# Optimization experiments

Hardware: AMD Instinct MI355X
Metric: run time of the kernel (lower is better)

## Reference

```python
import jax, jax.numpy as jnp
import numpy as np

GELU = lambda x: jax.nn.gelu(x, approximate=False)  # torch nn.GELU default (erf)
BN_EPS = 1e-5

def _conv(x, w, pad):
    return jax.lax.conv_general_dilated(x, w, (1, 1), pad,
                                        dimension_numbers=('NCHW', 'OIHW', 'NCHW'))

def setup_inputs() -> dict:
    B, D, L = 4096, 768, 3
    IC, R = D // 2, 16  # FDA intermediate channels, reduction ratio
    ks = iter(jax.random.split(jax.random.key(0), 64))
    def nrm(shape, s=0.02):
        return jax.random.normal(next(ks), shape, jnp.float32) * s
    z = lambda *s: jnp.zeros(s, jnp.float32)
    o = lambda *s: jnp.ones(s, jnp.float32)
    inp = {
        'text_feature': jax.random.normal(next(ks), (B, D), jnp.float32),
        'image_feature': jax.random.normal(next(ks), (B, D), jnp.float32),
        'tl_w': nrm((D, D)), 'tl_b': z(D),
        'il_w': nrm((D, D)), 'il_b': z(D),
        'sda_wq': nrm((512, D)), 'sda_bq': z(512),
        'sda_wk': nrm((512, D)), 'sda_bk': z(512),
        'sda_wv': nrm((512, D)), 'sda_bv': z(512),
        'sda_wo': nrm((D, 512)), 'sda_bo': z(D),
        'fda_w1': nrm((IC, D, 3, 3)), 'fda_b1': z(IC),
        'fda_bn1_g': o(IC), 'fda_bn1_b': z(IC),
        'fda_ca_w1': nrm((IC // R, IC, 1, 1)), 'fda_ca_w2': nrm((IC, IC // R, 1, 1)),
        'fda_sa_w': nrm((1, IC, 7, 7)), 'fda_sa_b': z(1),
        'fda_dec_w': nrm((1, IC, 1, 1)), 'fda_dec_b': z(1),
        'fda_sigma': jnp.full((1, IC, 1, 1), 1e-5, jnp.float32),
        'fda_wf': nrm((D, IC, 1, 1)), 'fda_bf': z(D),
        'fda_bn2_g': o(D), 'fda_bn2_b': z(D),
        'dmi_wq': nrm((D, D)), 'dmi_bq': z(D),
        'dmi_wk': nrm((D, D)), 'dmi_bk': z(D),
        'dmi_wv': nrm((D, D)), 'dmi_bv': z(D),
        'tg_w1': nrm((D, D)), 'tg_b1': z(D),
        'tg_w2': nrm((D, D)), 'tg_b2': z(D),
        'ig_w1': nrm((D, D)), 'ig_b1': z(D),
        'ig_w2': nrm((D, D)), 'ig_b2': z(D),
        'text_scale': o(1, D), 'image_scale': o(1, D),
        'cls_w': nrm((L, D)), 'cls_b': z(L),
    }
    return inp

def reference(text_feature, image_feature, tl_w, tl_b, il_w, il_b,
              sda_wq, sda_bq, sda_wk, sda_bk, sda_wv, sda_bv, sda_wo, sda_bo,
              fda_w1, fda_b1, fda_bn1_g, fda_bn1_b, fda_ca_w1, fda_ca_w2,
              fda_sa_w, fda_sa_b, fda_dec_w, fda_dec_b, fda_sigma,
              fda_wf, fda_bf, fda_bn2_g, fda_bn2_b,
              dmi_wq, dmi_bq, dmi_wk, dmi_bk, dmi_wv, dmi_bv,
              tg_w1, tg_b1, tg_w2, tg_b2, ig_w1, ig_b1, ig_w2, ig_b2,
              text_scale, image_scale, cls_w, cls_b):
    B, D = text_feature.shape
    H, DK = 8, 64
    # text/image projections (+GELU; dropout is identity at inference)
    t = GELU(text_feature @ tl_w.T + tl_b)
    im = GELU(image_feature @ il_w.T + il_b)
    # SDA multi-head self-attention on text, seq len 1
    q = (t @ sda_wq.T + sda_bq).reshape(B, 1, H, DK).transpose(0, 2, 1, 3)  # [B,H,1,DK]
    k = (t @ sda_wk.T + sda_bk).reshape(B, 1, H, DK).transpose(0, 2, 1, 3)
    v = (t @ sda_wv.T + sda_bv).reshape(B, 1, H, DK).transpose(0, 2, 1, 3)
    att = jax.nn.softmax(jnp.einsum('bhqd,bhkd->bhqk', q, k) / jnp.sqrt(jnp.float32(DK)), -1)
    t = jnp.einsum('bhqk,bhkd->bhqd', att, v).transpose(0, 2, 1, 3).reshape(B, H * DK) @ sda_wo.T + sda_bo
    # FDA on image feature viewed as [B,C,1,1]
    bnscale = 1.0 / jnp.sqrt(1.0 + BN_EPS)  # BN eval mode, running_mean=0, running_var=1
    x = im[:, :, None, None]
    x = _conv(x, fda_w1, ((1, 1), (1, 1))) + fda_b1[None, :, None, None]
    x = GELU(x * bnscale * fda_bn1_g[None, :, None, None] + fda_bn1_b[None, :, None, None])
    ca = jnp.mean(x, axis=(2, 3), keepdims=True)  # AdaptiveAvgPool2d(1)
    ca = GELU(_conv(ca, fda_ca_w1, ((0, 0), (0, 0))))
    ca = jax.nn.sigmoid(_conv(ca, fda_ca_w2, ((0, 0), (0, 0))))
    x = x * ca
    sa = jax.nn.sigmoid(_conv(x, fda_sa_w, ((3, 3), (3, 3))) + fda_sa_b[None, :, None, None])
    x = x * sa
    xg = GELU(_conv(x, fda_dec_w, ((0, 0), (0, 0))) + fda_dec_b[None, :, None, None])  # [B,1,1,1]
    x = x + fda_sigma * (x - xg)  # feat_decompose residual with learned sigma
    x = _conv(x, fda_wf, ((0, 0), (0, 0))) + fda_bf[None, :, None, None]
    x = GELU(x * bnscale * fda_bn2_g[None, :, None, None] + fda_bn2_b[None, :, None, None])
    im = x[:, :, 0, 0]

    def dmi(q_in, kv_in, gw1, gb1, gw2, gb2, scale):
        qp = q_in @ dmi_wq.T + dmi_bq
        kp = kv_in @ dmi_wk.T + dmi_bk
        vp = kv_in @ dmi_wv.T + dmi_bv
        # cross-batch attention: scores are [B,B]
        a = jax.nn.softmax(qp @ kp.T / jnp.sqrt(jnp.float32(D)), -1) @ vp
        # gate Sequential ends in Sigmoid, then forward applies sigmoid AGAIN (faithful)
        gate = jax.nn.sigmoid(jax.nn.relu(a @ gw1.T + gb1) @ gw2.T + gb2)
        return jax.nn.sigmoid(gate) * a * scale

    ct = dmi(t, im, tg_w1, tg_b1, tg_w2, tg_b2, text_scale)
    ci = dmi(im, t, ig_w1, ig_b1, ig_w2, ig_b2, image_scale)
    logits = (ct + ci) @ cls_w.T + cls_b
    return jax.nn.softmax(logits, -1)
```

## Files before the change

kernel.cpp:

```cpp
#include <hip/hip_runtime.h>
#include <hip/hip_bf16.h>
#include <math.h>

typedef __hip_bfloat16 bf16;
typedef __bf16 bf16x8 __attribute__((ext_vector_type(8)));
typedef float f32x4 __attribute__((ext_vector_type(4)));
typedef unsigned short u16;
typedef u16 u16x8 __attribute__((ext_vector_type(8)));

#define NB 4096
#define DM 768

__device__ __forceinline__ float cvt(float x){ return x; }
__device__ __forceinline__ float cvt(bf16 x){ return __bfloat162float(x); }
__device__ __forceinline__ void stv(float* p, float v){ *p = v; }
__device__ __forceinline__ void stv(bf16* p, float v){ *p = __float2bfloat16(v); }

__device__ __forceinline__ float gelu_f(float x){
    return 0.5f * x * (1.0f + erff(x * 0.70710678118654752440f));
}
__device__ __forceinline__ float sigmoid_f(float x){
    return 1.0f / (1.0f + expf(-x));
}

__device__ __forceinline__ void async_copy16(const void* g, void* l){
    __builtin_amdgcn_global_load_lds((const __attribute__((address_space(1))) void*)g,
                                     (__attribute__((address_space(3))) void*)l, 16, 0, 0);
}

#define MAXJ 8
struct Job {
    const bf16* A; const bf16* B; bf16* C;
    const float* b0; const float* gv; const float* b1;
    int M, N, K, ldA, ldB, act, trans, blk0, nx;
    float alpha;
};
struct Jobs { Job j[MAXJ]; int nj; };

__global__ __launch_bounds__(256) void mgemm_k(Jobs jb)
{
    int z = 0;
    #pragma unroll
    for (int i = 1; i < MAXJ; ++i)
        if (i < jb.nj && (int)blockIdx.x >= jb.j[i].blk0) z = i;
    const Job& J = jb.j[z];
    const bf16* __restrict__ A  = J.A;
    const bf16* __restrict__ Bm = J.B;
    bf16* __restrict__ C        = J.C;
    const int bx = (int)blockIdx.x - J.blk0;
    const int gx = bx % J.nx;
    const int gy = bx / J.nx;
    const int M = J.M, N = J.N, K = J.K, ldA = J.ldA, ldB = J.ldB;

    __shared__ __align__(16) bf16 Asl[128 * 32];
    __shared__ __align__(16) bf16 Bsl[128 * 32];
    const int tid  = threadIdx.x;
    const int wave = tid >> 6;
    const int lane = tid & 63;
    const int row0 = gy * 128;
    const int col0 = gx * 128;
    const int wrow = (wave & 1) * 64;
    const int wcol = (wave >> 1) * 64;
    const int fl   = lane & 15;
    const int srow = lane >> 2;
    const int scol = (((lane & 3) ^ ((lane >> 3) & 3))) * 8;
    const int ko2  = (((lane >> 4) ^ ((fl >> 1) & 3))) * 8;

    const bf16* pA = A  + (size_t)(row0 + wave * 32 + srow) * ldA + scol;
    const bf16* pB = Bm + (size_t)(col0 + wave * 32 + srow) * ldB + scol;
    bf16* ldsA = &Asl[(wave * 32) * 32];
    bf16* ldsB = &Bsl[(wave * 32) * 32];
    const size_t rstepA = (size_t)16 * ldA;
    const size_t rstepB = (size_t)16 * ldB;

    f32x4 acc[4][4] = {};
    for (int k0 = 0; k0 < K; k0 += 32){
        async_copy16(pA,          ldsA);
        async_copy16(pA + rstepA, ldsA + 16 * 32);
        async_copy16(pB,          ldsB);
        async_copy16(pB + rstepB, ldsB + 16 * 32);
        pA += 32; pB += 32;
        __syncthreads();
        bf16x8 af[4], bfv[4];
        #pragma unroll
        for (int i = 0; i < 4; ++i){
            af[i]  = *(const bf16x8*)&Asl[(wrow + i * 16 + fl) * 32 + ko2];
            bfv[i] = *(const bf16x8*)&Bsl[(wcol + i * 16 + fl) * 32 + ko2];
        }
        #pragma unroll
        for (int mi = 0; mi < 4; ++mi)
            #pragma unroll
            for (int ni = 0; ni < 4; ++ni)
                acc[mi][ni] = __builtin_amdgcn_mfma_f32_16x16x32_bf16(af[mi], bfv[ni], acc[mi][ni], 0, 0, 0);
        __syncthreads();
    }

    #pragma unroll
    for (int ni = 0; ni < 4; ++ni){
        const int col = col0 + wcol + ni * 16 + fl;
        const float b0 = J.b0 ? J.b0[col] : 0.f;
        const float gm = (J.gv ? J.gv[col] : 1.f) * J.alpha;
        const float b1 = J.b1 ? J.b1[col] : 0.f;
        #pragma unroll
        for (int mi = 0; mi < 4; ++mi){
            const int rbase = row0 + wrow + mi * 16 + (lane >> 4) * 4;
            #pragma unroll
            for (int r = 0; r < 4; ++r){
                float v = (acc[mi][ni][r] + b0) * gm + b1;
                if      (J.act == 1) v = gelu_f(v);
                else if (J.act == 2) v = sigmoid_f(v);
                else if (J.act == 3) v = fmaxf(v, 0.f);
                if (J.trans) stv(&C[(size_t)col * M + rbase + r], v);
                else         stv(&C[(size_t)(rbase + r) * N + col], v);
            }
        }
    }
}

#define NCVT 14
struct CvtDesc { const float* s[NCVT]; bf16* d[NCVT]; int n[NCVT]; };
__global__ __launch_bounds__(256) void cvt_k(CvtDesc cd)
{
    const int e = blockIdx.y;
    const int base = (blockIdx.x * 256 + threadIdx.x) * 4;
    if (base >= cd.n[e]) return;
    const float4 v = *(const float4*)(cd.s[e] + base);
    union { bf16 h[4]; unsigned long long u; } o;
    o.h[0] = __float2bfloat16(v.x);
    o.h[1] = __float2bfloat16(v.y);
    o.h[2] = __float2bfloat16(v.z);
    o.h[3] = __float2bfloat16(v.w);
    *(unsigned long long*)(cd.d[e] + base) = o.u;
}

__global__ __launch_bounds__(256) void extract_k(
    const float* __restrict__ w1, const float* __restrict__ saw,
    bf16* __restrict__ w1c, float* __restrict__ sac)
{
    const int idx = blockIdx.x * 256 + threadIdx.x;
    if (idx < 384 * 768){
        const int oc = idx / 768, ic = idx % 768;
        w1c[idx] = __float2bfloat16(w1[(size_t)oc * 6912 + (size_t)ic * 9 + 4]);
    }
    if (idx < 384) sac[idx] = saw[(size_t)idx * 49 + 24];
}

__global__ __launch_bounds__(128) void fda_fused_k(
    bf16* __restrict__ x, const float* __restrict__ wc1, const float* __restrict__ wc2,
    const float* __restrict__ sac, const float* __restrict__ sab,
    const float* __restrict__ decw, const float* __restrict__ decb,
    const float* __restrict__ sigma)
{
    __shared__ float xs[384];
    __shared__ float ca1s[24];
    __shared__ float red[128];
    const int b = blockIdx.x;
    const int tid = threadIdx.x;
    bf16* xr = x + (size_t)b * 384;
    #pragma unroll
    for (int i = 0; i < 3; ++i) xs[tid + i * 128] = cvt(xr[tid + i * 128]);
    __syncthreads();
    if (tid < 96){
        const int o = tid >> 2, sub = tid & 3;
        const float* w = wc1 + (size_t)o * 384 + sub * 96;
        float p = 0.f;
        #pragma unroll 8
        for (int k = 0; k < 96; ++k) p = fmaf(xs[sub * 96 + k], w[k], p);
        p += __shfl_down(p, 1, 64);
        p += __shfl_down(p, 2, 64);
        if (sub == 0) ca1s[o] = gelu_f(p);
    }
    __syncthreads();
    float x2[3];
    float p = 0.f;
    #pragma unroll
    for (int i = 0; i < 3; ++i){
        const int c = tid + i * 128;
        float s = 0.f;
        const float* w = wc2 + (size_t)c * 24;
        #pragma unroll
        for (int k = 0; k < 24; ++k) s = fmaf(ca1s[k], w[k], s);
        const float v = xs[c] * sigmoid_f(s);
        x2[i] = v;
        p += v * sac[c];
    }
    red[tid] = p; __syncthreads();
    for (int s = 64; s > 0; s >>= 1){ if (tid < s) red[tid] += red[tid + s]; __syncthreads(); }
    const float sa = sigmoid_f(red[0] + sab[0]);
    __syncthreads();
    float q = 0.f;
    #pragma unroll
    for (int i = 0; i < 3; ++i){
        const int c = tid + i * 128;
        x2[i] *= sa;
        q += x2[i] * decw[c];
    }
    red[tid] = q; __syncthreads();
    for (int s = 64; s > 0; s >>= 1){ if (tid < s) red[tid] += red[tid + s]; __syncthreads(); }
    const float xg = gelu_f(red[0] + decb[0]);
    #pragma unroll
    for (int i = 0; i < 3; ++i){
        const int c = tid + i * 128;
        const float sg = sigma[c];
        stv(&xr[c], x2[i] + sg * (x2[i] - xg));
    }
}

__global__ __launch_bounds__(256) void softmax_rows_k(bf16* __restrict__ S)
{
    __shared__ float red[256];
    const int tid = threadIdx.x;
    u16* r = (u16*)(S + (size_t)blockIdx.x * NB) + tid * 16;
    u16x8 h0 = *(const u16x8*)r;
    u16x8 h1 = *(const u16x8*)(r + 8);
    float v[16];
    #pragma unroll
    for (int i = 0; i < 8; ++i){
        v[i]     = __uint_as_float((unsigned)h0[i] << 16);
        v[8 + i] = __uint_as_float((unsigned)h1[i] << 16);
    }
    float m = v[0];
    #pragma unroll
    for (int i = 1; i < 16; ++i) m = fmaxf(m, v[i]);
    red[tid] = m; __syncthreads();
    for (int s = 128; s > 0; s >>= 1){ if (tid < s) red[tid] = fmaxf(red[tid], red[tid + s]); __syncthreads(); }
    m = red[0]; __syncthreads();
    float sum = 0.f;
    #pragma unroll
    for (int i = 0; i < 16; ++i){ v[i] = expf(v[i] - m); sum += v[i]; }
    red[tid] = sum; __syncthreads();
    for (int s = 128; s > 0; s >>= 1){ if (tid < s) red[tid] += red[tid + s]; __syncthreads(); }
    const float inv = 1.0f / red[0];
    u16x8 o0, o1;
    #pragma unroll
    for (int i = 0; i < 8; ++i){
        o0[i] = __bfloat16_as_ushort(__float2bfloat16(v[i] * inv));
        o1[i] = __bfloat16_as_ushort(__float2bfloat16(v[8 + i] * inv));
    }
    *(u16x8*)r = o0;
    *(u16x8*)(r + 8) = o1;
}

__global__ __launch_bounds__(256) void reduce2_k(
    const bf16* __restrict__ a, const bf16* __restrict__ b, bf16* __restrict__ o1,
    const bf16* __restrict__ c, const bf16* __restrict__ d, bf16* __restrict__ o2)
{
    const size_t i = ((size_t)blockIdx.x * 256 + threadIdx.x) * 8;
    if (i >= (size_t)NB * DM) return;
    u16x8 ua = *(const u16x8*)((const u16*)a + i);
    u16x8 ub = *(const u16x8*)((const u16*)b + i);
    u16x8 uc = *(const u16x8*)((const u16*)c + i);
    u16x8 ud = *(const u16x8*)((const u16*)d + i);
    u16x8 r1, r2;
    #pragma unroll
    for (int j = 0; j < 8; ++j){
        const float s1 = __uint_as_float((unsigned)ua[j] << 16) + __uint_as_float((unsigned)ub[j] << 16);
        const float s2 = __uint_as_float((unsigned)uc[j] << 16) + __uint_as_float((unsigned)ud[j] << 16);
        r1[j] = __bfloat16_as_ushort(__float2bfloat16(s1));
        r2[j] = __bfloat16_as_ushort(__float2bfloat16(s2));
    }
    *(u16x8*)((u16*)o1 + i) = r1;
    *(u16x8*)((u16*)o2 + i) = r2;
}

__global__ __launch_bounds__(256) void combine2_k(
    bf16* __restrict__ acc,
    const bf16* __restrict__ g1, const bf16* __restrict__ a1, const float* __restrict__ s1,
    const bf16* __restrict__ g2, const bf16* __restrict__ a2, const float* __restrict__ s2)
{
    const size_t idx = (size_t)blockIdx.x * 256 + threadIdx.x;
    if (idx >= (size_t)NB * DM) return;
    const int col = (int)(idx % DM);
    const float v = sigmoid_f(cvt(g1[idx])) * cvt(a1[idx]) * s1[col]
                  + sigmoid_f(cvt(g2[idx])) * cvt(a2[idx]) * s2[col];
    stv(&acc[idx], v);
}

__global__ __launch_bounds__(64) void cls_softmax_k(
    const bf16* __restrict__ acc, const float* __restrict__ w,
    const float* __restrict__ bias, float* __restrict__ out)
{
    const int b = blockIdx.x;
    const bf16* r = acc + (size_t)b * DM;
    float p0 = 0.f, p1 = 0.f, p2 = 0.f;
    for (int k = threadIdx.x; k < DM; k += 64){
        const float v = cvt(r[k]);
        p0 = fmaf(v, w[k],        p0);
        p1 = fmaf(v, w[DM + k],   p1);
        p2 = fmaf(v, w[2*DM + k], p2);
    }
    #pragma unroll
    for (int off = 32; off > 0; off >>= 1){
        p0 += __shfl_down(p0, off, 64);
        p1 += __shfl_down(p1, off, 64);
        p2 += __shfl_down(p2, off, 64);
    }
    if (threadIdx.x == 0){
        const float l0 = p0 + bias[0];
        const float l1 = p1 + bias[1];
        const float l2 = p2 + bias[2];
        const float mx = fmaxf(l0, fmaxf(l1, l2));
        const float e0 = expf(l0 - mx), e1 = expf(l1 - mx), e2 = expf(l2 - mx);
        const float inv = 1.f / (e0 + e1 + e2);
        out[(size_t)b * 3 + 0] = e0 * inv;
        out[(size_t)b * 3 + 1] = e1 * inv;
        out[(size_t)b * 3 + 2] = e2 * inv;
    }
}

extern "C" void kernel_launch(void* const* d_in, const int* in_sizes, int n_in,
                              void* d_out, int out_size, void* d_ws, size_t ws_size,
                              hipStream_t stream)
{
    const float* text   = (const float*)d_in[0];
    const float* image  = (const float*)d_in[1];
    const float* tl_w   = (const float*)d_in[2];
    const float* tl_b   = (const float*)d_in[3];
    const float* il_w   = (const float*)d_in[4];
    const float* il_b   = (const float*)d_in[5];
    const float* sda_wv = (const float*)d_in[10];
    const float* sda_bv = (const float*)d_in[11];
    const float* sda_wo = (const float*)d_in[12];
    const float* sda_bo = (const float*)d_in[13];
    const float* fda_w1 = (const float*)d_in[14];
    const float* fda_b1 = (const float*)d_in[15];
    const float* bn1_g  = (const float*)d_in[16];
    const float* bn1_b  = (const float*)d_in[17];
    const float* ca_w1  = (const float*)d_in[18];
    const float* ca_w2  = (const float*)d_in[19];
    const float* sa_w   = (const float*)d_in[20];
    const float* sa_b   = (const float*)d_in[21];
    const float* dec_w  = (const float*)d_in[22];
    const float* dec_b  = (const float*)d_in[23];
    const float* sigma  = (const float*)d_in[24];
    const float* fda_wf = (const float*)d_in[25];
    const float* fda_bf = (const float*)d_in[26];
    const float* bn2_g  = (const float*)d_in[27];
    const float* bn2_b  = (const float*)d_in[28];
    const float* dmi_wq = (const float*)d_in[29];
    const float* dmi_bq = (const float*)d_in[30];
    const float* dmi_wk = (const float*)d_in[31];
    const float* dmi_bk = (const float*)d_in[32];
    const float* dmi_wv = (const float*)d_in[33];
    const float* dmi_bv = (const float*)d_in[34];
    const float* tg_w1  = (const float*)d_in[35];
    const float* tg_b1  = (const float*)d_in[36];
    const float* tg_w2  = (const float*)d_in[37];
    const float* tg_b2  = (const float*)d_in[38];
    const float* ig_w1  = (const float*)d_in[39];
    const float* ig_b1  = (const float*)d_in[40];
    const float* ig_w2  = (const float*)d_in[41];
    const float* ig_b2  = (const float*)d_in[42];
    const float* t_scale= (const float*)d_in[43];
    const float* i_scale= (const float*)d_in[44];
    const float* cls_w  = (const float*)d_in[45];
    const float* cls_b  = (const float*)d_in[46];
    float* out = (float*)d_out;

    char* base = (char*)d_ws;
    auto alloc = [&](size_t bytes){ void* p = (void*)base; base += (bytes + 255) & ~(size_t)255; return p; };
    const size_t SLOT = (size_t)NB * DM;
    const size_t W768 = (size_t)768 * 768;
    bf16* tl_wb   = (bf16*)alloc(W768 * 2);
    bf16* il_wb   = (bf16*)alloc(W768 * 2);
    bf16* sda_wvb = (bf16*)alloc((size_t)512 * 768 * 2);
    bf16* sda_wob = (bf16*)alloc((size_t)768 * 512 * 2);
    bf16* fda_wfb = (bf16*)alloc((size_t)768 * 384 * 2);
    bf16* dmi_wqb = (bf16*)alloc(W768 * 2);
    bf16* dmi_wkb = (bf16*)alloc(W768 * 2);
    bf16* dmi_wvb = (bf16*)alloc(W768 * 2);
    bf16* tg_w1b  = (bf16*)alloc(W768 * 2);
    bf16* tg_w2b  = (bf16*)alloc(W768 * 2);
    bf16* ig_w1b  = (bf16*)alloc(W768 * 2);
    bf16* ig_w2b  = (bf16*)alloc(W768 * 2);
    bf16* w1c     = (bf16*)alloc((size_t)384 * 768 * 2);
    float* sac    = (float*)alloc(1536 * 4);
    bf16* SL[8];
    for (int i = 0; i < 8; ++i) SL[i] = (bf16*)alloc(SLOT * 2);
    bf16* SC1 = (bf16*)alloc((size_t)NB * NB * 2);
    bf16* SC2 = (bf16*)alloc((size_t)NB * NB * 2);

    const float bnscale = 1.0f / sqrtf(1.0f + 1e-5f);
    const float iscale  = 1.0f / sqrtf(768.0f);
    const dim3 blk(256);

    struct JB {
        Jobs jb; int blocks;
        void add(const bf16* A, const bf16* B, bf16* C, int M, int N, int K, int ldA, int ldB,
                 const float* b0, float al, const float* gv, const float* b1, int act, int trans){
            Job& j = jb.j[jb.nj++];
            j.A=A; j.B=B; j.C=C; j.b0=b0; j.gv=gv; j.b1=b1;
            j.M=M; j.N=N; j.K=K; j.ldA=ldA; j.ldB=ldB; j.act=act; j.trans=trans;
            j.alpha=al; j.blk0=blocks; j.nx=N/128;
            blocks += (N/128)*(M/128);
        }
    };
    auto launch = [&](JB& b){ mgemm_k<<<dim3(b.blocks), blk, 0, stream>>>(b.jb); };

    CvtDesc cd;
    const float* srcs[NCVT] = {text, image, tl_w, il_w, sda_wv, sda_wo, fda_wf,
                               dmi_wq, dmi_wk, dmi_wv, tg_w1, tg_w2, ig_w1, ig_w2};
    bf16* dsts[NCVT] = {SL[0], SL[1], tl_wb, il_wb, sda_wvb, sda_wob, fda_wfb,
                        dmi_wqb, dmi_wkb, dmi_wvb, tg_w1b, tg_w2b, ig_w1b, ig_w2b};
    int   lens[NCVT] = {(int)SLOT, (int)SLOT, (int)W768, (int)W768, 512*768, 768*512, 768*384,
                        (int)W768, (int)W768, (int)W768, (int)W768, (int)W768, (int)W768, (int)W768};
    for (int i = 0; i < NCVT; ++i){ cd.s[i] = srcs[i]; cd.d[i] = dsts[i]; cd.n[i] = lens[i]; }
    cvt_k<<<dim3((int)(SLOT / 1024), NCVT), blk, 0, stream>>>(cd);
    extract_k<<<dim3((384 * 768 + 255) / 256), blk, 0, stream>>>(fda_w1, sa_w, w1c, sac);

    { JB b{}; b.add(SL[0], tl_wb, SL[2], NB, DM, DM, DM, DM, tl_b, 1.f, nullptr, nullptr, 1, 0);
              b.add(SL[1], il_wb, SL[3], NB, DM, DM, DM, DM, il_b, 1.f, nullptr, nullptr, 1, 0); launch(b); }
    { JB b{}; b.add(SL[2], sda_wvb, SL[0], NB, 512, DM, DM, DM, sda_bv, 1.f, nullptr, nullptr, 0, 0);
              b.add(SL[3], w1c,     SL[1], NB, 384, DM, DM, DM, fda_b1, bnscale, bn1_g, bn1_b, 1, 0); launch(b); }
    { JB b{}; b.add(SL[0], sda_wob, SL[4], NB, DM, 512, 512, 512, sda_bo, 1.f, nullptr, nullptr, 0, 0); launch(b); }
    fda_fused_k<<<dim3(NB), dim3(128), 0, stream>>>(SL[1], ca_w1, ca_w2, sac, sa_b, dec_w, dec_b, sigma);
    { JB b{}; b.add(SL[1], fda_wfb, SL[5], NB, DM, 384, 384, 384, fda_bf, bnscale, bn2_g, bn2_b, 1, 0); launch(b); }

    { JB b{};
      b.add(SL[4], dmi_wqb, SL[0], NB, DM, DM, DM, DM, dmi_bq, 1.f, nullptr, nullptr, 0, 0);
      b.add(SL[5], dmi_wkb, SL[1], NB, DM, DM, DM, DM, dmi_bk, 1.f, nullptr, nullptr, 0, 0);
      b.add(SL[5], dmi_wvb, SL[2], NB, DM, DM, DM, DM, dmi_bv, 1.f, nullptr, nullptr, 0, 1);
      b.add(SL[5], dmi_wqb, SL[3], NB, DM, DM, DM, DM, dmi_bq, 1.f, nullptr, nullptr, 0, 0);
      b.add(SL[4], dmi_wkb, SL[6], NB, DM, DM, DM, DM, dmi_bk, 1.f, nullptr, nullptr, 0, 0);
      b.add(SL[4], dmi_wvb, SL[7], NB, DM, DM, DM, DM, dmi_bv, 1.f, nullptr, nullptr, 0, 1);
      launch(b); }
    { JB b{}; b.add(SL[0], SL[1], SC1, NB, NB, DM, DM, DM, nullptr, iscale, nullptr, nullptr, 0, 0);
              b.add(SL[3], SL[6], SC2, NB, NB, DM, DM, DM, nullptr, iscale, nullptr, nullptr, 0, 0); launch(b); }
    softmax_rows_k<<<dim3(2 * NB), blk, 0, stream>>>(SC1);
    { JB b{};
      b.add(SC1,        SL[2],        SL[0], NB, DM, 2048, NB, NB, nullptr, 1.f, nullptr, nullptr, 0, 0);
      b.add(SC1 + 2048, SL[2] + 2048, SL[1], NB, DM, 2048, NB, NB, nullptr, 1.f, nullptr, nullptr, 0, 0);
      b.add(SC2,        SL[7],        SL[3], NB, DM, 2048, NB, NB, nullptr, 1.f, nullptr, nullptr, 0, 0);
      b.add(SC2 + 2048, SL[7] + 2048, SL[6], NB, DM, 2048, NB, NB, nullptr, 1.f, nullptr, nullptr, 0, 0);
      launch(b); }
    reduce2_k<<<dim3((int)(SLOT / 2048)), blk, 0, stream>>>(SL[0], SL[1], SL[4], SL[3], SL[6], SL[5]);
    { JB b{}; b.add(SL[4], tg_w1b, SL[0], NB, DM, DM, DM, DM, tg_b1, 1.f, nullptr, nullptr, 3, 0);
              b.add(SL[5], ig_w1b, SL[1], NB, DM, DM, DM, DM, ig_b1, 1.f, nullptr, nullptr, 3, 0); launch(b); }
    { JB b{}; b.add(SL[0], tg_w2b, SL[3], NB, DM, DM, DM, DM, tg_b2, 1.f, nullptr, nullptr, 2, 0);
              b.add(SL[1], ig_w2b, SL[6], NB, DM, DM, DM, DM, ig_b2, 1.f, nullptr, nullptr, 2, 0); launch(b); }
    combine2_k<<<dim3((NB * DM + 255) / 256), blk, 0, stream>>>(SL[2], SL[3], SL[4], t_scale, SL[6], SL[5], i_scale);
    cls_softmax_k<<<dim3(NB), dim3(64), 0, stream>>>(SL[2], cls_w, cls_b, out);
}
```

Baseline: 657.4 us.

## Use BK=64 tiles with XOR swizzle and stage GEMM epilogue through LDS

The batched bf16 GEMM kernel now loads K-tiles of 64 instead of 32, with an 8-way XOR swizzle. This halves the number of barrier pairs per K loop and gives two MFMA sub-steps per tile. The epilogue writes the activated results into a padded shared-memory tile and then stores them to global memory as 16-byte vectors. This replaces scattered 2-byte stores, which matters most for the transposed output case. Shared memory grows to about 34 KB per block, which may lower occupancy, and the epilogue adds an extra LDS round trip.

```diff
diff --git a/kernel.cpp b/kernel.cpp
--- a/kernel.cpp
+++ b/kernel.cpp
@@ -52,8 +52,7 @@
     const int gy = bx / J.nx;
     const int M = J.M, N = J.N, K = J.K, ldA = J.ldA, ldB = J.ldB;
 
-    __shared__ __align__(16) bf16 Asl[128 * 32];
-    __shared__ __align__(16) bf16 Bsl[128 * 32];
+    __shared__ __align__(16) bf16 smem[17408];
     const int tid  = threadIdx.x;
     const int wave = tid >> 6;
     const int lane = tid & 63;
@@ -62,58 +61,76 @@
     const int wrow = (wave & 1) * 64;
     const int wcol = (wave >> 1) * 64;
     const int fl   = lane & 15;
-    const int srow = lane >> 2;
-    const int scol = (((lane & 3) ^ ((lane >> 3) & 3))) * 8;
-    const int ko2  = (((lane >> 4) ^ ((fl >> 1) & 3))) * 8;
-
-    const bf16* pA = A  + (size_t)(row0 + wave * 32 + srow) * ldA + scol;
-    const bf16* pB = Bm + (size_t)(col0 + wave * 32 + srow) * ldB + scol;
-    bf16* ldsA = &Asl[(wave * 32) * 32];
-    bf16* ldsB = &Bsl[(wave * 32) * 32];
-    const size_t rstepA = (size_t)16 * ldA;
-    const size_t rstepB = (size_t)16 * ldB;
+    const int q    = lane >> 4;
+
+    const int sr8 = lane >> 3;
+    const int sc8 = (((lane & 7) ^ sr8)) * 8;
+    const bf16* pA = A  + (size_t)(row0 + wave * 32 + sr8) * ldA + sc8;
+    const bf16* pB = Bm + (size_t)(col0 + wave * 32 + sr8) * ldB + sc8;
+    bf16* ldsA = &smem[(wave * 32) * 64];
+    bf16* ldsB = &smem[8192 + (wave * 32) * 64];
 
     f32x4 acc[4][4] = {};
-    for (int k0 = 0; k0 < K; k0 += 32){
-        async_copy16(pA,          ldsA);
-        async_copy16(pA + rstepA, ldsA + 16 * 32);
-        async_copy16(pB,          ldsB);
-        async_copy16(pB + rstepB, ldsB + 16 * 32);
-        pA += 32; pB += 32;
-        __syncthreads();
-        bf16x8 af[4], bfv[4];
+    for (int k0 = 0; k0 < K; k0 += 64){
         #pragma unroll
         for (int i = 0; i < 4; ++i){
-            af[i]  = *(const bf16x8*)&Asl[(wrow + i * 16 + fl) * 32 + ko2];
-            bfv[i] = *(const bf16x8*)&Bsl[(wcol + i * 16 + fl) * 32 + ko2];
+            async_copy16(pA + (size_t)(i * 8) * ldA, ldsA + i * 512);
+            async_copy16(pB + (size_t)(i * 8) * ldB, ldsB + i * 512);
         }
+        pA += 64; pB += 64;
+        __syncthreads();
         #pragma unroll
-        for (int mi = 0; mi < 4; ++mi)
+        for (int ks = 0; ks < 2; ++ks){
+            bf16x8 af[4], bfv[4];
             #pragma unroll
-            for (int ni = 0; ni < 4; ++ni)
-                acc[mi][ni] = __builtin_amdgcn_mfma_f32_16x16x32_bf16(af[mi], bfv[ni], acc[mi][ni], 0, 0, 0);
+            for (int i = 0; i < 4; ++i){
+                const int ra = wrow + i * 16 + fl;
+                const int rb = wcol + i * 16 + fl;
+                const int ca = ((ks * 4 + q) ^ (ra & 7)) * 8;
+                const int cb = ((ks * 4 + q) ^ (rb & 7)) * 8;
+                af[i]  = *(const bf16x8*)&smem[ra * 64 + ca];
+                bfv[i] = *(const bf16x8*)&smem[8192 + rb * 64 + cb];
+            }
+            #pragma unroll
+            for (int mi = 0; mi < 4; ++mi)
+                #pragma unroll
+                for (int ni = 0; ni < 4; ++ni)
+                    acc[mi][ni] = __builtin_amdgcn_mfma_f32_16x16x32_bf16(af[mi], bfv[ni], acc[mi][ni], 0, 0, 0);
+        }
         __syncthreads();
     }
 
+    constexpr int ELD = 136;
     #pragma unroll
     for (int ni = 0; ni < 4; ++ni){
         const int col = col0 + wcol + ni * 16 + fl;
         const float b0 = J.b0 ? J.b0[col] : 0.f;
         const float gm = (J.gv ? J.gv[col] : 1.f) * J.alpha;
         const float b1 = J.b1 ? J.b1[col] : 0.f;
+        const int lcol = wcol + ni * 16 + fl;
         #pragma unroll
         for (int mi = 0; mi < 4; ++mi){
-            const int rbase = row0 + wrow + mi * 16 + (lane >> 4) * 4;
+            const int lrow = wrow + mi * 16 + q * 4;
             #pragma unroll
             for (int r = 0; r < 4; ++r){
                 float v = (acc[mi][ni][r] + b0) * gm + b1;
                 if      (J.act == 1) v = gelu_f(v);
                 else if (J.act == 2) v = sigmoid_f(v);
                 else if (J.act == 3) v = fmaxf(v, 0.f);
-                if (J.trans) stv(&C[(size_t)col * M + rbase + r], v);
-                else         stv(&C[(size_t)(rbase + r) * N + col], v);
+                if (J.trans) smem[(size_t)lcol * ELD + lrow + r] = __float2bfloat16(v);
+                else         smem[(size_t)(lrow + r) * ELD + lcol] = __float2bfloat16(v);
             }
         }
+    }
+    __syncthreads();
+    const int erow = tid >> 4;
+    const int ecol = (tid & 15) * 8;
+    #pragma unroll
+    for (int p = 0; p < 8; ++p){
+        const int row = p * 16 + erow;
+        const bf16x8 val = *(const bf16x8*)&smem[row * ELD + ecol];
+        if (J.trans) *(bf16x8*)&C[(size_t)(col0 + row) * M + row0 + ecol] = val;
+        else         *(bf16x8*)&C[(size_t)(row0 + row) * N + col0 + ecol] = val;
     }
 }
 
@@ -188,14 +205,14 @@
     for (int s = 64; s > 0; s >>= 1){ if (tid < s) red[tid] += red[tid + s]; __syncthreads(); }
     const float sa = sigmoid_f(red[0] + sab[0]);
     __syncthreads();
-    float q = 0.f;
+    float qq = 0.f;
     #pragma unroll
     for (int i = 0; i < 3; ++i){
         const int c = tid + i * 128;
         x2[i] *= sa;
-        q += x2[i] * decw[c];
-    }
-    red[tid] = q; __syncthreads();
+        qq += x2[i] * decw[c];
+    }
+    red[tid] = qq; __syncthreads();
     for (int s = 64; s > 0; s >>= 1){ if (tid < s) red[tid] += red[tid + s]; __syncthreads(); }
     const float xg = gelu_f(red[0] + decb[0]);
     #pragma unroll
```

After: 600.4 us. -8.7%, faster.
